# Kernel tuning notes

Measured on AMD Instinct MI355X. Metric: run time of the kernel, lower is better.

Reference implementation:

```python
import jax, jax.numpy as jnp
import numpy as np

B, S, H = 2, 1024, 4096
NH, DH, NKV = 32, 128, 2          # heads, head_dim, kv groups
ROT = DH // 2                      # 64: GLM rotates first half of head dim
GROUP = NH // NKV                  # 16 query heads per kv group
SCALE = DH ** -0.5


def glm_rope(x, pos):
    """GLM interleaved rotary on first ROT dims. x: [B,S,h,DH], pos: [B,S] int."""
    rot, rest = x[..., :ROT], x[..., ROT:]
    inv_freq = 1.0 / (10000.0 ** (jnp.arange(0, ROT, 2, dtype=jnp.float32) / ROT))  # [ROT/2]
    ang = pos.astype(jnp.float32)[:, :, None] * inv_freq[None, None, :]             # [B,S,ROT/2]
    cos = jnp.cos(ang)[:, :, None, :]
    sin = jnp.sin(ang)[:, :, None, :]
    x0, x1 = rot[..., 0::2], rot[..., 1::2]
    o0 = x0 * cos - x1 * sin
    o1 = x1 * cos + x0 * sin
    rot_out = jnp.stack([o0, o1], axis=-1).reshape(rot.shape)
    return jnp.concatenate([rot_out, rest], axis=-1)


def setup_inputs() -> dict:
    key = jax.random.key(0)
    k1, k2, k3, k4 = jax.random.split(key, 4)
    return {
        "hidden_states": jax.random.normal(k1, (B, S, H), jnp.float32) * 0.02,
        "position_ids": jnp.arange(B * S, dtype=jnp.int32).reshape(B, S) % S,
        "W_qkv": jax.random.normal(k2, (H, NH * DH + 2 * NKV * DH), jnp.float32) * 0.02,
        "b_qkv": jax.random.normal(k3, (NH * DH + 2 * NKV * DH,), jnp.float32) * 0.02,
        "W_dense": jax.random.normal(k4, (NH * DH, H), jnp.float32) * 0.02,
    }


def reference(hidden_states, position_ids, W_qkv, b_qkv, W_dense):
    qkv = hidden_states @ W_qkv + b_qkv                              # [B,S,4608]
    q = qkv[..., : NH * DH].reshape(B, S, NH, DH)
    k = qkv[..., NH * DH : NH * DH + NKV * DH].reshape(B, S, NKV, DH)
    v = qkv[..., NH * DH + NKV * DH :].reshape(B, S, NKV, DH)

    q = glm_rope(q, position_ids)
    k = glm_rope(k, position_ids)

    # GQA: expand kv groups to all heads
    k = jnp.repeat(k, GROUP, axis=2)                                 # [B,S,NH,DH]
    v = jnp.repeat(v, GROUP, axis=2)

    scores = jnp.einsum("bqhd,bkhd->bhqk", q, k) * SCALE             # [B,NH,S,S]
    causal = jnp.tril(jnp.ones((S, S), dtype=bool))
    scores = jnp.where(causal[None, None], scores, jnp.finfo(scores.dtype).min)
    probs = jax.nn.softmax(scores, axis=-1)
    ctx = jnp.einsum("bhqk,bkhd->bqhd", probs, v).reshape(B, S, NH * DH)
    return ctx @ W_dense                                             # [B,S,H]
```

## Files before the change

kernel.cpp:

```cpp
#include <hip/hip_runtime.h>

#define B_    2
#define S_    1024
#define H_    4096
#define NH_   32
#define DH_   128
#define NKV_  2
#define GROUP_ 16
#define ROT_  64
#define NQKV_ 4608
#define SCALE_ 0.08838834764831845f
#define KVB   64

typedef __attribute__((ext_vector_type(8))) short bf16x8;
typedef __attribute__((ext_vector_type(4))) float f32x4;

typedef __attribute__((address_space(1))) const void* gptr_t;
typedef __attribute__((address_space(3))) void* lptr_t;

__device__ __forceinline__ unsigned short f2bf(float f) {
    unsigned int u = __builtin_bit_cast(unsigned int, f);
    u += 0x7FFFu + ((u >> 16) & 1u);
    return (unsigned short)(u >> 16);
}
__device__ __forceinline__ unsigned int pack2bf(float a, float b) {
    return (unsigned int)f2bf(a) | ((unsigned int)f2bf(b) << 16);
}

__global__ void k_f32_to_bf16(const float* __restrict__ in,
                              unsigned short* __restrict__ out, int n4) {
    int i = blockIdx.x * blockDim.x + threadIdx.x;
    if (i >= n4) return;
    const float4 v = reinterpret_cast<const float4*>(in)[i];
    ushort4 o;
    o.x = f2bf(v.x); o.y = f2bf(v.y); o.z = f2bf(v.z); o.w = f2bf(v.w);
    reinterpret_cast<ushort4*>(out)[i] = o;
}

__global__ void k_transpose_bf16(const float* __restrict__ in,
                                 unsigned short* __restrict__ out,
                                 int K, int N) {
    __shared__ float tile[32][33];
    const int n0 = blockIdx.x * 32, k0 = blockIdx.y * 32;
    const int tx = threadIdx.x, ty = threadIdx.y;
    for (int j = ty; j < 32; j += 8)
        tile[j][tx] = in[(size_t)(k0 + j) * N + n0 + tx];
    __syncthreads();
    for (int j = ty; j < 32; j += 8)
        out[(size_t)(n0 + j) * K + k0 + tx] = f2bf(tile[tx][j]);
}

__global__ __launch_bounds__(512) void k_gemm_bt(
    const unsigned short* __restrict__ A,
    const unsigned short* __restrict__ Bt,
    const float* __restrict__ bias,
    float* __restrict__ Cf,
    int M, int N, int K)
{
    __shared__ __align__(16) char lds[2][49152];

    const int tid  = threadIdx.x;
    const int wave = tid >> 6, lane = tid & 63;
    const int lrow = lane & 15, lhi = lane >> 4;
    const int wm = (wave >> 2) * 64;
    const int wn = (wave & 3) * 64;
    const size_t a_row0 = (size_t)blockIdx.y * 128;
    const size_t b_col0 = (size_t)blockIdx.x * 256;

    const size_t strideA = (size_t)K * 2;
    const char* Abase = (const char*)A + (a_row0 + wave * 8 + (lane >> 3)) * strideA;
    const char* Bbase = (const char*)Bt + (b_col0 + wave * 8 + (lane >> 3)) * strideA;
    const int swz_src = ((lane & 7) * 16) ^ (((lane >> 3) & 7) << 4);
    const int lds_off = wave * 1024 + lane * 16;

    f32x4 acc[4][4] = {};

    const int nt = K >> 6;

    {
        const int kb = 0;
        #pragma unroll
        for (int j = 0; j < 2; j++)
            __builtin_amdgcn_global_load_lds(
                (gptr_t)(Abase + (size_t)j * 64 * strideA + kb + swz_src),
                (lptr_t)(lds[0] + j * 8192 + lds_off), 16, 0, 0);
        #pragma unroll
        for (int j = 0; j < 4; j++)
            __builtin_amdgcn_global_load_lds(
                (gptr_t)(Bbase + (size_t)j * 64 * strideA + kb + swz_src),
                (lptr_t)(lds[0] + 16384 + j * 8192 + lds_off), 16, 0, 0);
    }
    asm volatile("s_waitcnt vmcnt(0)" ::: "memory");
    __builtin_amdgcn_s_barrier();

    int cur = 0;
    for (int t = 0; t < nt; t++) {
        if (t + 1 < nt) {
            const int kb = (t + 1) * 128;
            #pragma unroll
            for (int j = 0; j < 2; j++)
                __builtin_amdgcn_global_load_lds(
                    (gptr_t)(Abase + (size_t)j * 64 * strideA + kb + swz_src),
                    (lptr_t)(lds[cur ^ 1] + j * 8192 + lds_off), 16, 0, 0);
            #pragma unroll
            for (int j = 0; j < 4; j++)
                __builtin_amdgcn_global_load_lds(
                    (gptr_t)(Bbase + (size_t)j * 64 * strideA + kb + swz_src),
                    (lptr_t)(lds[cur ^ 1] + 16384 + j * 8192 + lds_off), 16, 0, 0);
        }
        const char* La = lds[cur];
        const char* Lb = lds[cur] + 16384;
        bf16x8 af[4][2], bf[4][2];
        #pragma unroll
        for (int i = 0; i < 4; i++) {
            const int fr = wm + i * 16 + lrow;
            #pragma unroll
            for (int ks = 0; ks < 2; ks++)
                af[i][ks] = *(const bf16x8*)(
                    La + fr * 128 + ((ks * 64 + lhi * 16) ^ ((lrow & 7) << 4)));
        }
        #pragma unroll
        for (int j = 0; j < 4; j++) {
            const int br = wn + j * 16 + lrow;
            #pragma unroll
            for (int ks = 0; ks < 2; ks++)
                bf[j][ks] = *(const bf16x8*)(
                    Lb + br * 128 + ((ks * 64 + lhi * 16) ^ ((lrow & 7) << 4)));
        }
        __builtin_amdgcn_s_setprio(1);
        #pragma unroll
        for (int i = 0; i < 4; i++)
            #pragma unroll
            for (int j = 0; j < 4; j++) {
                acc[i][j] = __builtin_amdgcn_mfma_f32_16x16x32_bf16(
                    af[i][0], bf[j][0], acc[i][j], 0, 0, 0);
                acc[i][j] = __builtin_amdgcn_mfma_f32_16x16x32_bf16(
                    af[i][1], bf[j][1], acc[i][j], 0, 0, 0);
            }
        __builtin_amdgcn_s_setprio(0);
        asm volatile("s_waitcnt vmcnt(0)" ::: "memory");
        __builtin_amdgcn_s_barrier();
        cur ^= 1;
    }

    #pragma unroll
    for (int i = 0; i < 4; i++)
        #pragma unroll
        for (int j = 0; j < 4; j++) {
            const size_t grow0 = a_row0 + wm + i * 16 + lhi * 4;
            const size_t gcol  = b_col0 + wn + j * 16 + lrow;
            const float bi = bias ? bias[gcol] : 0.f;
            #pragma unroll
            for (int r = 0; r < 4; r++)
                Cf[(grow0 + r) * N + gcol] = acc[i][j][r] + bi;
        }
}

__global__ void k_rope_reorg(const float* __restrict__ qkv,
                             const int* __restrict__ pos_ids,
                             unsigned short* __restrict__ Qh,
                             unsigned short* __restrict__ Kh,
                             unsigned short* __restrict__ Vt)
{
    const int NPR = (NH_ + 2 * NKV_) * 64;
    const int idx = blockIdx.x * blockDim.x + threadIdx.x;
    if (idx >= B_ * S_ * NPR) return;
    const int t = idx / NPR;
    const int rem = idx % NPR;
    const int unit = rem >> 6;
    const int pr = rem & 63;
    const int b = t >> 10, s = t & 1023;
    const float pos = (float)pos_ids[t];
    const float* row = qkv + (size_t)t * NQKV_;

    if (unit < NH_) {
        const int col = unit * DH_ + 2 * pr;
        float x0 = row[col], x1 = row[col + 1];
        if (pr < 32) {
            const float ang = pos * powf(10000.f, -(float)pr / 32.f);
            float sn, cs; sincosf(ang, &sn, &cs);
            const float o0 = x0 * cs - x1 * sn;
            const float o1 = x1 * cs + x0 * sn;
            x0 = o0; x1 = o1;
        }
        unsigned short* dst = Qh + ((size_t)((b * NH_ + unit) * S_) + s) * DH_ + 2 * pr;
        dst[0] = f2bf(x0); dst[1] = f2bf(x1);
    } else if (unit < NH_ + NKV_) {
        const int g = unit - NH_;
        const int col = NH_ * DH_ + g * DH_ + 2 * pr;
        float x0 = row[col], x1 = row[col + 1];
        if (pr < 32) {
            const float ang = pos * powf(10000.f, -(float)pr / 32.f);
            float sn, cs; sincosf(ang, &sn, &cs);
            const float o0 = x0 * cs - x1 * sn;
            const float o1 = x1 * cs + x0 * sn;
            x0 = o0; x1 = o1;
        }
        unsigned short* dst = Kh + ((size_t)((b * NKV_ + g) * S_) + s) * DH_ + 2 * pr;
        dst[0] = f2bf(x0); dst[1] = f2bf(x1);
    } else {
        const int g = unit - NH_ - NKV_;
        const int col = NH_ * DH_ + NKV_ * DH_ + g * DH_ + 2 * pr;
        const float x0 = row[col], x1 = row[col + 1];
        unsigned short* d0 = Vt + ((size_t)((b * NKV_ + g) * DH_) + 2 * pr) * S_ + s;
        d0[0]  = f2bf(x0);
        d0[S_] = f2bf(x1);
    }
}

__global__ __launch_bounds__(256) void k_attn(
    const unsigned short* __restrict__ Qh,
    const unsigned short* __restrict__ Kh,
    const unsigned short* __restrict__ Vt,
    unsigned short* __restrict__ ctx)
{
    __shared__ __align__(16) char lds_kt[2][16384];
    __shared__ __align__(16) char lds_vt[16384];
    __shared__ __align__(16) char lds_p[4][2048];

    const int tid  = threadIdx.x;
    const int wave = tid >> 6, lane = tid & 63;
    const int lrow = lane & 15, lhi = lane >> 4;
    char* myp = lds_p[wave];

    const int blk  = blockIdx.x;
    const int pair = blk & 7;
    const int h    = (blk >> 3) & 31;
    const int b    = blk >> 8;
    const int g    = h >> 4;

    const char* Kbase = (const char*)(Kh + (size_t)((b * NKV_ + g) * S_) * DH_);
    const char* Vbase = (const char*)(Vt + (size_t)((b * NKV_ + g) * DH_) * S_);

    const int kcol = lrow * 16;
    const int vrow_l = lane >> 3;
    const int vcol = (lane & 7) * 16;

    for (int half = 0; half < 2; half++) {
        const int qt = half ? (15 - pair) : pair;
        const int q0 = qt * 64 + wave * 16;
        const int ntiles = qt + 1;
        const int q_glob = q0 + lrow;

        #pragma unroll
        for (int i = 0; i < 4; i++) {
            const int ci = wave * 4 + i;
            const int r  = ci * 4 + lhi;
            __builtin_amdgcn_global_load_lds(
                (gptr_t)(Kbase + (size_t)r * 256 + (kcol ^ ((r & 7) << 4))),
                (lptr_t)(lds_kt[0] + ci * 1024), 16, 0, 0);
        }
        const unsigned short* Qp = Qh + ((size_t)((b * NH_ + h) * S_) + q0) * DH_;
        bf16x8 a_q[4];
        #pragma unroll
        for (int ks = 0; ks < 4; ks++)
            a_q[ks] = *(const bf16x8*)(Qp + (size_t)lrow * DH_ + ks * 32 + lhi * 8);
        asm volatile("s_waitcnt vmcnt(0)" ::: "memory");
        __builtin_amdgcn_s_barrier();

        float m_run = -1e30f, l_run = 0.f;
        f32x4 o_acc[8] = {};
        int cur = 0;

        for (int t = 0; t < ntiles; t++) {
            const bool has_next = (t + 1 < ntiles);
            #pragma unroll
            for (int i = 0; i < 4; i++) {
                const int ci = wave * 4 + i;
                const int r  = ci * 8 + vrow_l;
                __builtin_amdgcn_global_load_lds(
                    (gptr_t)(Vbase + (size_t)r * (S_ * 2) + t * (KVB * 2)
                             + (vcol ^ ((r & 7) << 4))),
                    (lptr_t)(lds_vt + ci * 1024), 16, 0, 0);
            }
            if (has_next) {
                const char* ksrc = Kbase + (size_t)(t + 1) * 16384;
                #pragma unroll
                for (int i = 0; i < 4; i++) {
                    const int ci = wave * 4 + i;
                    const int r  = ci * 4 + lhi;
                    __builtin_amdgcn_global_load_lds(
                        (gptr_t)(ksrc + (size_t)r * 256 + (kcol ^ ((r & 7) << 4))),
                        (lptr_t)(lds_kt[cur ^ 1] + ci * 1024), 16, 0, 0);
                }
            }
            f32x4 s_acc[4] = {};
            #pragma unroll
            for (int sub = 0; sub < 4; sub++) {
                const int r = sub * 16 + lrow;
                #pragma unroll
                for (int ks = 0; ks < 4; ks++) {
                    const bf16x8 a_k = *(const bf16x8*)(
                        lds_kt[cur] + r * 256 + ((ks * 64 + lhi * 16) ^ ((r & 7) << 4)));
                    s_acc[sub] = __builtin_amdgcn_mfma_f32_16x16x32_bf16(
                        a_k, a_q[ks], s_acc[sub], 0, 0, 0);
                }
            }
            float pv[16];
            float mx = -1e30f;
            if (!has_next) {
                #pragma unroll
                for (int sub = 0; sub < 4; sub++)
                    #pragma unroll
                    for (int r = 0; r < 4; r++) {
                        const int kvg = t * KVB + sub * 16 + lhi * 4 + r;
                        float sv = s_acc[sub][r] * SCALE_;
                        if (kvg > q_glob) sv = -1e30f;
                        pv[sub * 4 + r] = sv;
                        mx = fmaxf(mx, sv);
                    }
            } else {
                #pragma unroll
                for (int sub = 0; sub < 4; sub++)
                    #pragma unroll
                    for (int r = 0; r < 4; r++) {
                        const float sv = s_acc[sub][r] * SCALE_;
                        pv[sub * 4 + r] = sv;
                        mx = fmaxf(mx, sv);
                    }
            }
            mx = fmaxf(mx, __shfl_xor(mx, 16));
            mx = fmaxf(mx, __shfl_xor(mx, 32));
            const float mnew = fmaxf(m_run, mx);
            const float scale = __expf(m_run - mnew);
            m_run = mnew;
            float sm = 0.f;
            #pragma unroll
            for (int i = 0; i < 16; i++) {
                const float e = __expf(pv[i] - mnew);
                pv[i] = e;
                sm += e;
            }
            sm += __shfl_xor(sm, 16);
            sm += __shfl_xor(sm, 32);
            l_run = l_run * scale + sm;
            #pragma unroll
            for (int d = 0; d < 8; d++) {
                o_acc[d][0] *= scale; o_acc[d][1] *= scale;
                o_acc[d][2] *= scale; o_acc[d][3] *= scale;
            }
            #pragma unroll
            for (int sub = 0; sub < 4; sub++) {
                const int off = (lrow * 128 + sub * 32 + lhi * 8) ^ ((lrow & 7) << 4);
                *reinterpret_cast<uint2*>(myp + off) = make_uint2(
                    pack2bf(pv[sub * 4 + 0], pv[sub * 4 + 1]),
                    pack2bf(pv[sub * 4 + 2], pv[sub * 4 + 3]));
            }
            bf16x8 a_p[2];
            #pragma unroll
            for (int frag = 0; frag < 2; frag++) {
                const int off = (lrow * 128 + frag * 64 + lhi * 16) ^ ((lrow & 7) << 4);
                a_p[frag] = *reinterpret_cast<const bf16x8*>(myp + off);
            }
            if (has_next) asm volatile("s_waitcnt vmcnt(4)" ::: "memory");
            else          asm volatile("s_waitcnt vmcnt(0)" ::: "memory");
            __builtin_amdgcn_s_barrier();
            #pragma unroll
            for (int d = 0; d < 8; d++) {
                const int r = d * 16 + lrow;
                #pragma unroll
                for (int frag = 0; frag < 2; frag++) {
                    const bf16x8 a_v = *(const bf16x8*)(
                        lds_vt + r * 128 + ((frag * 64 + lhi * 16) ^ ((r & 7) << 4)));
                    o_acc[d] = __builtin_amdgcn_mfma_f32_16x16x32_bf16(
                        a_v, a_p[frag], o_acc[d], 0, 0, 0);
                }
            }
            asm volatile("s_waitcnt vmcnt(0)" ::: "memory");
            __builtin_amdgcn_s_barrier();
            cur ^= 1;
        }
        const float inv = 1.f / l_run;
        const size_t row = (size_t)b * S_ + q0 + lrow;
        #pragma unroll
        for (int d = 0; d < 8; d++) {
            unsigned short* dst = ctx + row * (NH_ * DH_) + h * DH_ + d * 16 + lhi * 4;
            *reinterpret_cast<uint2*>(dst) = make_uint2(
                pack2bf(o_acc[d][0] * inv, o_acc[d][1] * inv),
                pack2bf(o_acc[d][2] * inv, o_acc[d][3] * inv));
        }
    }
}

extern "C" void kernel_launch(void* const* d_in, const int* in_sizes, int n_in,
                              void* d_out, int out_size, void* d_ws, size_t ws_size,
                              hipStream_t stream)
{
    const float* hidden  = (const float*)d_in[0];
    const int*   pos_ids = (const int*)d_in[1];
    const float* W_qkv   = (const float*)d_in[2];
    const float* b_qkv   = (const float*)d_in[3];
    const float* W_dense = (const float*)d_in[4];
    float* out = (float*)d_out;

    char* ws = (char*)d_ws;
    unsigned short* Xbf = (unsigned short*)(ws);
    unsigned short* Wqt = (unsigned short*)(ws + 16777216);
    unsigned short* Wdt = (unsigned short*)(ws + 54525952);
    float*          qkv = (float*)         (ws + 88080384);
    unsigned short* Qh  = (unsigned short*)(ws + 125829120);
    unsigned short* Kh  = (unsigned short*)(ws + 142606336);
    unsigned short* Vt  = (unsigned short*)(ws + 143654912);
    unsigned short* Ctx = (unsigned short*)(ws + 144703488);

    const int M = B_ * S_;

    k_f32_to_bf16<<<(M * H_ / 4 + 255) / 256, 256, 0, stream>>>(hidden, Xbf, M * H_ / 4);
    dim3 tb(32, 8);
    k_transpose_bf16<<<dim3(NQKV_ / 32, H_ / 32), tb, 0, stream>>>(W_qkv, Wqt, H_, NQKV_);
    k_transpose_bf16<<<dim3(H_ / 32, H_ / 32), tb, 0, stream>>>(W_dense, Wdt, H_, H_);
    k_gemm_bt<<<dim3(NQKV_ / 256, M / 128), 512, 0, stream>>>(
        Xbf, Wqt, b_qkv, qkv, M, NQKV_, H_);
    k_rope_reorg<<<(M * 2304 + 255) / 256, 256, 0, stream>>>(qkv, pos_ids, Qh, Kh, Vt);
    k_attn<<<B_ * NH_ * 8, 256, 0, stream>>>(Qh, Kh, Vt, Ctx);
    k_gemm_bt<<<dim3(H_ / 256, M / 128), 512, 0, stream>>>(
        Ctx, Wdt, nullptr, out, M, H_, H_);
}
```

Measured before the change: 331.4 us.

## Use 256x256 GEMM tiles with XCD-aware block remap and finer-grained waits

Replaces the 128x256 GEMM with a 256x256 tile in which each wave accumulates 8x4 MFMA fragments. Blocks are launched on a 1D grid and remapped so that consecutive blocks on the same XCD share operand tiles, aiming at better L2 reuse. The pipeline now waits only for the previous prefetch batch (vmcnt(8)) before its barrier, and adds barriers between A sub-panels inside each K step. Doubling the tile halves the block count: 144 blocks for the QKV GEMM and 128 for the dense GEMM, fewer than the chip's CUs. Each block also uses 128 KB of LDS, so the larger tile trades occupancy and parallelism for operand reuse.

```diff
diff --git a/kernel.cpp b/kernel.cpp
--- a/kernel.cpp
+++ b/kernel.cpp
@@ -50,109 +50,109 @@
         out[(size_t)(n0 + j) * K + k0 + tx] = f2bf(tile[tx][j]);
 }
 
-__global__ __launch_bounds__(512) void k_gemm_bt(
+__global__ __launch_bounds__(512) void k_gemm8(
     const unsigned short* __restrict__ A,
     const unsigned short* __restrict__ Bt,
     const float* __restrict__ bias,
     float* __restrict__ Cf,
-    int M, int N, int K)
+    int N, int K, int gx)
 {
-    __shared__ __align__(16) char lds[2][49152];
+    __shared__ __align__(16) char lds[2][65536];
 
     const int tid  = threadIdx.x;
     const int wave = tid >> 6, lane = tid & 63;
     const int lrow = lane & 15, lhi = lane >> 4;
-    const int wm = (wave >> 2) * 64;
-    const int wn = (wave & 3) * 64;
-    const size_t a_row0 = (size_t)blockIdx.y * 128;
-    const size_t b_col0 = (size_t)blockIdx.x * 256;
-
-    const size_t strideA = (size_t)K * 2;
-    const char* Abase = (const char*)A + (a_row0 + wave * 8 + (lane >> 3)) * strideA;
-    const char* Bbase = (const char*)Bt + (b_col0 + wave * 8 + (lane >> 3)) * strideA;
+    const int wm = wave >> 2, wn = wave & 3;
+
+    const int id = blockIdx.x;
+    const int cm = (id & 7) * gx + (id >> 3);
+    const int bcol = cm >> 3, brow = cm & 7;
+    const size_t a_row0 = (size_t)brow * 256;
+    const size_t b_col0 = (size_t)bcol * 256;
+
+    const size_t strideK = (size_t)K * 2;
+    const char* Asrc = (const char*)A + (a_row0 + wave * 8 + (lane >> 3)) * strideK;
+    const char* Bsrc = (const char*)Bt + (b_col0 + wave * 8 + (lane >> 3)) * strideK;
     const int swz_src = ((lane & 7) * 16) ^ (((lane >> 3) & 7) << 4);
-    const int lds_off = wave * 1024 + lane * 16;
-
-    f32x4 acc[4][4] = {};
-
+    const int dst_off = wave * 1024 + lane * 16;
+
+    f32x4 acc[8][4] = {};
     const int nt = K >> 6;
 
-    {
-        const int kb = 0;
-        #pragma unroll
-        for (int j = 0; j < 2; j++)
-            __builtin_amdgcn_global_load_lds(
-                (gptr_t)(Abase + (size_t)j * 64 * strideA + kb + swz_src),
-                (lptr_t)(lds[0] + j * 8192 + lds_off), 16, 0, 0);
-        #pragma unroll
-        for (int j = 0; j < 4; j++)
-            __builtin_amdgcn_global_load_lds(
-                (gptr_t)(Bbase + (size_t)j * 64 * strideA + kb + swz_src),
-                (lptr_t)(lds[0] + 16384 + j * 8192 + lds_off), 16, 0, 0);
+    #pragma unroll
+    for (int j = 0; j < 4; j++) {
+        __builtin_amdgcn_global_load_lds(
+            (gptr_t)(Asrc + (size_t)j * 64 * strideK + swz_src),
+            (lptr_t)(lds[0] + j * 8192 + dst_off), 16, 0, 0);
+        __builtin_amdgcn_global_load_lds(
+            (gptr_t)(Bsrc + (size_t)j * 64 * strideK + swz_src),
+            (lptr_t)(lds[0] + 32768 + j * 8192 + dst_off), 16, 0, 0);
     }
-    asm volatile("s_waitcnt vmcnt(0)" ::: "memory");
-    __builtin_amdgcn_s_barrier();
 
     int cur = 0;
+    const int swz = (lrow & 7) << 4;
     for (int t = 0; t < nt; t++) {
         if (t + 1 < nt) {
-            const int kb = (t + 1) * 128;
-            #pragma unroll
-            for (int j = 0; j < 2; j++)
+            const size_t kb = (size_t)(t + 1) * 128;
+            #pragma unroll
+            for (int j = 0; j < 4; j++) {
                 __builtin_amdgcn_global_load_lds(
-                    (gptr_t)(Abase + (size_t)j * 64 * strideA + kb + swz_src),
-                    (lptr_t)(lds[cur ^ 1] + j * 8192 + lds_off), 16, 0, 0);
-            #pragma unroll
-            for (int j = 0; j < 4; j++)
+                    (gptr_t)(Asrc + (size_t)j * 64 * strideK + kb + swz_src),
+                    (lptr_t)(lds[cur ^ 1] + j * 8192 + dst_off), 16, 0, 0);
                 __builtin_amdgcn_global_load_lds(
-                    (gptr_t)(Bbase + (size_t)j * 64 * strideA + kb + swz_src),
-                    (lptr_t)(lds[cur ^ 1] + 16384 + j * 8192 + lds_off), 16, 0, 0);
-        }
+                    (gptr_t)(Bsrc + (size_t)j * 64 * strideK + kb + swz_src),
+                    (lptr_t)(lds[cur ^ 1] + 32768 + j * 8192 + dst_off), 16, 0, 0);
+            }
+            asm volatile("s_waitcnt vmcnt(8)" ::: "memory");
+        } else {
+            asm volatile("s_waitcnt vmcnt(0)" ::: "memory");
+        }
+        __builtin_amdgcn_s_barrier();
+
         const char* La = lds[cur];
-        const char* Lb = lds[cur] + 16384;
-        bf16x8 af[4][2], bf[4][2];
-        #pragma unroll
-        for (int i = 0; i < 4; i++) {
-            const int fr = wm + i * 16 + lrow;
-            #pragma unroll
-            for (int ks = 0; ks < 2; ks++)
-                af[i][ks] = *(const bf16x8*)(
-                    La + fr * 128 + ((ks * 64 + lhi * 16) ^ ((lrow & 7) << 4)));
-        }
-        #pragma unroll
-        for (int j = 0; j < 4; j++) {
-            const int br = wn + j * 16 + lrow;
-            #pragma unroll
-            for (int ks = 0; ks < 2; ks++)
-                bf[j][ks] = *(const bf16x8*)(
-                    Lb + br * 128 + ((ks * 64 + lhi * 16) ^ ((lrow & 7) << 4)));
-        }
-        __builtin_amdgcn_s_setprio(1);
-        #pragma unroll
-        for (int i = 0; i < 4; i++)
-            #pragma unroll
-            for (int j = 0; j < 4; j++) {
-                acc[i][j] = __builtin_amdgcn_mfma_f32_16x16x32_bf16(
-                    af[i][0], bf[j][0], acc[i][j], 0, 0, 0);
-                acc[i][j] = __builtin_amdgcn_mfma_f32_16x16x32_bf16(
-                    af[i][1], bf[j][1], acc[i][j], 0, 0, 0);
-            }
-        __builtin_amdgcn_s_setprio(0);
-        asm volatile("s_waitcnt vmcnt(0)" ::: "memory");
-        __builtin_amdgcn_s_barrier();
+        const char* Lb = lds[cur] + 32768;
+        bf16x8 bfr[4][2];
+        #pragma unroll
+        for (int n = 0; n < 4; n++) {
+            const int r = wn * 64 + n * 16 + lrow;
+            bfr[n][0] = *(const bf16x8*)(Lb + r * 128 + ((lhi * 16) ^ swz));
+            bfr[n][1] = *(const bf16x8*)(Lb + r * 128 + ((64 + lhi * 16) ^ swz));
+        }
+        #pragma unroll
+        for (int p = 0; p < 4; p++) {
+            bf16x8 af[2][2];
+            #pragma unroll
+            for (int i = 0; i < 2; i++) {
+                const int r = wm * 128 + (p * 2 + i) * 16 + lrow;
+                af[i][0] = *(const bf16x8*)(La + r * 128 + ((lhi * 16) ^ swz));
+                af[i][1] = *(const bf16x8*)(La + r * 128 + ((64 + lhi * 16) ^ swz));
+            }
+            __builtin_amdgcn_s_setprio(1);
+            #pragma unroll
+            for (int i = 0; i < 2; i++)
+                #pragma unroll
+                for (int n = 0; n < 4; n++) {
+                    acc[p * 2 + i][n] = __builtin_amdgcn_mfma_f32_16x16x32_bf16(
+                        af[i][0], bfr[n][0], acc[p * 2 + i][n], 0, 0, 0);
+                    acc[p * 2 + i][n] = __builtin_amdgcn_mfma_f32_16x16x32_bf16(
+                        af[i][1], bfr[n][1], acc[p * 2 + i][n], 0, 0, 0);
+                }
+            __builtin_amdgcn_s_setprio(0);
+            __builtin_amdgcn_s_barrier();
+        }
         cur ^= 1;
     }
 
     #pragma unroll
-    for (int i = 0; i < 4; i++)
-        #pragma unroll
-        for (int j = 0; j < 4; j++) {
-            const size_t grow0 = a_row0 + wm + i * 16 + lhi * 4;
-            const size_t gcol  = b_col0 + wn + j * 16 + lrow;
+    for (int m = 0; m < 8; m++)
+        #pragma unroll
+        for (int n = 0; n < 4; n++) {
+            const size_t grow0 = a_row0 + wm * 128 + m * 16 + lhi * 4;
+            const size_t gcol  = b_col0 + wn * 64 + n * 16 + lrow;
             const float bi = bias ? bias[gcol] : 0.f;
             #pragma unroll
             for (int r = 0; r < 4; r++)
-                Cf[(grow0 + r) * N + gcol] = acc[i][j][r] + bi;
+                Cf[(grow0 + r) * N + gcol] = acc[m][n][r] + bi;
         }
 }
 
@@ -409,10 +409,10 @@
     dim3 tb(32, 8);
     k_transpose_bf16<<<dim3(NQKV_ / 32, H_ / 32), tb, 0, stream>>>(W_qkv, Wqt, H_, NQKV_);
     k_transpose_bf16<<<dim3(H_ / 32, H_ / 32), tb, 0, stream>>>(W_dense, Wdt, H_, H_);
-    k_gemm_bt<<<dim3(NQKV_ / 256, M / 128), 512, 0, stream>>>(
-        Xbf, Wqt, b_qkv, qkv, M, NQKV_, H_);
+    k_gemm8<<<dim3((NQKV_ / 256) * 8), 512, 0, stream>>>(
+        Xbf, Wqt, b_qkv, qkv, NQKV_, H_, NQKV_ / 256);
     k_rope_reorg<<<(M * 2304 + 255) / 256, 256, 0, stream>>>(qkv, pos_ids, Qh, Kh, Vt);
     k_attn<<<B_ * NH_ * 8, 256, 0, stream>>>(Qh, Kh, Vt, Ctx);
-    k_gemm_bt<<<dim3(H_ / 256, M / 128), 512, 0, stream>>>(
-        Ctx, Wdt, nullptr, out, M, H_, H_);
-}
+    k_gemm8<<<dim3((H_ / 256) * 8), 512, 0, stream>>>(
+        Ctx, Wdt, nullptr, out, H_, H_, H_ / 256);
+}
```

After: 383.5 us. 1.16x slower.

## Shrink GEMM tile to 128x128 with 256 threads and partial vmcnt waits

Applied to the files above, without the earlier changes.

Reworks the bf16 GEMM from a 128x256 block tile with 8 waves to a 128x128 tile with 4 waves and two blocks per CU. The wait on the next-tile prefetch moves to the top of the loop as a partial vmcnt(8) wait before the barrier, so that tile's loads stay in flight during compute. setprio is dropped. More blocks raise grid parallelism and occupancy on the many CUs, at the cost of more redundant global traffic per output element and an extra barrier each iteration.

```diff
diff --git a/kernel.cpp b/kernel.cpp
--- a/kernel.cpp
+++ b/kernel.cpp
@@ -50,95 +50,84 @@
         out[(size_t)(n0 + j) * K + k0 + tx] = f2bf(tile[tx][j]);
 }
 
-__global__ __launch_bounds__(512) void k_gemm_bt(
+__global__ __launch_bounds__(256, 2) void k_gemm_bt(
     const unsigned short* __restrict__ A,
     const unsigned short* __restrict__ Bt,
     const float* __restrict__ bias,
     float* __restrict__ Cf,
     int M, int N, int K)
 {
-    __shared__ __align__(16) char lds[2][49152];
+    __shared__ __align__(16) char lds[2][32768];
 
     const int tid  = threadIdx.x;
     const int wave = tid >> 6, lane = tid & 63;
     const int lrow = lane & 15, lhi = lane >> 4;
-    const int wm = (wave >> 2) * 64;
-    const int wn = (wave & 3) * 64;
+    const int wm = (wave >> 1) * 64, wn = (wave & 1) * 64;
     const size_t a_row0 = (size_t)blockIdx.y * 128;
-    const size_t b_col0 = (size_t)blockIdx.x * 256;
-
-    const size_t strideA = (size_t)K * 2;
-    const char* Abase = (const char*)A + (a_row0 + wave * 8 + (lane >> 3)) * strideA;
-    const char* Bbase = (const char*)Bt + (b_col0 + wave * 8 + (lane >> 3)) * strideA;
-    const int swz_src = ((lane & 7) * 16) ^ (((lane >> 3) & 7) << 4);
-    const int lds_off = wave * 1024 + lane * 16;
+    const size_t b_col0 = (size_t)blockIdx.x * 128;
+
+    const size_t strideK = (size_t)K * 2;
+    const char* Asrc = (const char*)A + (a_row0 + (tid >> 3)) * strideK;
+    const char* Bsrc = (const char*)Bt + (b_col0 + (tid >> 3)) * strideK;
+    const int swz_src = ((tid & 7) * 16) ^ (((tid >> 3) & 7) << 4);
+    const int dst_off = tid * 16;
 
     f32x4 acc[4][4] = {};
-
     const int nt = K >> 6;
 
-    {
-        const int kb = 0;
-        #pragma unroll
-        for (int j = 0; j < 2; j++)
-            __builtin_amdgcn_global_load_lds(
-                (gptr_t)(Abase + (size_t)j * 64 * strideA + kb + swz_src),
-                (lptr_t)(lds[0] + j * 8192 + lds_off), 16, 0, 0);
-        #pragma unroll
-        for (int j = 0; j < 4; j++)
-            __builtin_amdgcn_global_load_lds(
-                (gptr_t)(Bbase + (size_t)j * 64 * strideA + kb + swz_src),
-                (lptr_t)(lds[0] + 16384 + j * 8192 + lds_off), 16, 0, 0);
+    #pragma unroll
+    for (int j = 0; j < 4; j++) {
+        __builtin_amdgcn_global_load_lds(
+            (gptr_t)(Asrc + (size_t)j * 32 * strideK + swz_src),
+            (lptr_t)(lds[0] + j * 4096 + dst_off), 16, 0, 0);
+        __builtin_amdgcn_global_load_lds(
+            (gptr_t)(Bsrc + (size_t)j * 32 * strideK + swz_src),
+            (lptr_t)(lds[0] + 16384 + j * 4096 + dst_off), 16, 0, 0);
     }
-    asm volatile("s_waitcnt vmcnt(0)" ::: "memory");
-    __builtin_amdgcn_s_barrier();
 
     int cur = 0;
     for (int t = 0; t < nt; t++) {
         if (t + 1 < nt) {
-            const int kb = (t + 1) * 128;
-            #pragma unroll
-            for (int j = 0; j < 2; j++)
+            const size_t kb = (size_t)(t + 1) * 128;
+            #pragma unroll
+            for (int j = 0; j < 4; j++) {
                 __builtin_amdgcn_global_load_lds(
-                    (gptr_t)(Abase + (size_t)j * 64 * strideA + kb + swz_src),
-                    (lptr_t)(lds[cur ^ 1] + j * 8192 + lds_off), 16, 0, 0);
-            #pragma unroll
-            for (int j = 0; j < 4; j++)
+                    (gptr_t)(Asrc + (size_t)j * 32 * strideK + kb + swz_src),
+                    (lptr_t)(lds[cur ^ 1] + j * 4096 + dst_off), 16, 0, 0);
                 __builtin_amdgcn_global_load_lds(
-                    (gptr_t)(Bbase + (size_t)j * 64 * strideA + kb + swz_src),
-                    (lptr_t)(lds[cur ^ 1] + 16384 + j * 8192 + lds_off), 16, 0, 0);
-        }
+                    (gptr_t)(Bsrc + (size_t)j * 32 * strideK + kb + swz_src),
+                    (lptr_t)(lds[cur ^ 1] + 16384 + j * 4096 + dst_off), 16, 0, 0);
+            }
+            asm volatile("s_waitcnt vmcnt(8)" ::: "memory");
+        } else {
+            asm volatile("s_waitcnt vmcnt(0)" ::: "memory");
+        }
+        __builtin_amdgcn_s_barrier();
+
         const char* La = lds[cur];
         const char* Lb = lds[cur] + 16384;
-        bf16x8 af[4][2], bf[4][2];
+        bf16x8 af[4][2], bfr[4][2];
         #pragma unroll
         for (int i = 0; i < 4; i++) {
             const int fr = wm + i * 16 + lrow;
-            #pragma unroll
-            for (int ks = 0; ks < 2; ks++)
-                af[i][ks] = *(const bf16x8*)(
-                    La + fr * 128 + ((ks * 64 + lhi * 16) ^ ((lrow & 7) << 4)));
+            af[i][0] = *(const bf16x8*)(La + fr * 128 + ((lhi * 16) ^ ((fr & 7) << 4)));
+            af[i][1] = *(const bf16x8*)(La + fr * 128 + ((64 + lhi * 16) ^ ((fr & 7) << 4)));
         }
         #pragma unroll
         for (int j = 0; j < 4; j++) {
             const int br = wn + j * 16 + lrow;
-            #pragma unroll
-            for (int ks = 0; ks < 2; ks++)
-                bf[j][ks] = *(const bf16x8*)(
-                    Lb + br * 128 + ((ks * 64 + lhi * 16) ^ ((lrow & 7) << 4)));
-        }
-        __builtin_amdgcn_s_setprio(1);
+            bfr[j][0] = *(const bf16x8*)(Lb + br * 128 + ((lhi * 16) ^ ((br & 7) << 4)));
+            bfr[j][1] = *(const bf16x8*)(Lb + br * 128 + ((64 + lhi * 16) ^ ((br & 7) << 4)));
+        }
         #pragma unroll
         for (int i = 0; i < 4; i++)
             #pragma unroll
             for (int j = 0; j < 4; j++) {
                 acc[i][j] = __builtin_amdgcn_mfma_f32_16x16x32_bf16(
-                    af[i][0], bf[j][0], acc[i][j], 0, 0, 0);
+                    af[i][0], bfr[j][0], acc[i][j], 0, 0, 0);
                 acc[i][j] = __builtin_amdgcn_mfma_f32_16x16x32_bf16(
-                    af[i][1], bf[j][1], acc[i][j], 0, 0, 0);
-            }
-        __builtin_amdgcn_s_setprio(0);
-        asm volatile("s_waitcnt vmcnt(0)" ::: "memory");
+                    af[i][1], bfr[j][1], acc[i][j], 0, 0, 0);
+            }
         __builtin_amdgcn_s_barrier();
         cur ^= 1;
     }
@@ -409,10 +398,10 @@
     dim3 tb(32, 8);
     k_transpose_bf16<<<dim3(NQKV_ / 32, H_ / 32), tb, 0, stream>>>(W_qkv, Wqt, H_, NQKV_);
     k_transpose_bf16<<<dim3(H_ / 32, H_ / 32), tb, 0, stream>>>(W_dense, Wdt, H_, H_);
-    k_gemm_bt<<<dim3(NQKV_ / 256, M / 128), 512, 0, stream>>>(
+    k_gemm_bt<<<dim3(NQKV_ / 128, M / 128), 256, 0, stream>>>(
         Xbf, Wqt, b_qkv, qkv, M, NQKV_, H_);
     k_rope_reorg<<<(M * 2304 + 255) / 256, 256, 0, stream>>>(qkv, pos_ids, Qh, Kh, Vt);
     k_attn<<<B_ * NH_ * 8, 256, 0, stream>>>(Qh, Kh, Vt, Ctx);
-    k_gemm_bt<<<dim3(H_ / 256, M / 128), 512, 0, stream>>>(
+    k_gemm_bt<<<dim3(H_ / 128, M / 128), 256, 0, stream>>>(
         Ctx, Wdt, nullptr, out, M, H_, H_);
 }
```

Result: faster. 305.8 us (-7.7%).
